# Kernel optimization log

Measured on AMD Instinct MI355X. Metric: run time of the kernel, lower is better.

## Reference

```python
import jax, jax.numpy as jnp
import numpy as np
from jax import lax

H = 1024; E = 512; V = 32000; WIN_D = 10.0; PAD = 0
S_LEN = 64; T_LEN = 64; B = 32


def _lstm_cell(x, h, c, W_ih, W_hh, b):
    z = x @ W_ih.T + h @ W_hh.T + b  # [B,4H], torch gate order i,f,g,o
    i, f, g, o = jnp.split(z, 4, axis=-1)
    c2 = jax.nn.sigmoid(f) * c + jax.nn.sigmoid(i) * jnp.tanh(g)
    h2 = jax.nn.sigmoid(o) * jnp.tanh(c2)
    return h2, c2


def setup_inputs() -> dict:
    key = jax.random.key(0)
    ks = jax.random.split(key, 24)
    sc = 0.05
    rn = lambda k, shape: (jax.random.normal(k, shape, jnp.float32) * sc)
    src_tokens = jax.random.randint(ks[0], (S_LEN, B), 0, V, dtype=jnp.int32)
    tgt_tokens = jax.random.randint(ks[1], (T_LEN, B), 1, V, dtype=jnp.int32)
    encode_len = jax.random.randint(ks[2], (B,), S_LEN // 2, S_LEN + 1, dtype=jnp.int32)
    encode_len = encode_len.at[0].set(S_LEN)  # pad_packed pads to max len
    return {
        "src_tokens": src_tokens, "tgt_tokens": tgt_tokens, "encode_len": encode_len,
        "emb_src": rn(ks[3], (V, E)), "emb_tar": rn(ks[4], (V, E)),
        "eW_ih0": rn(ks[5], (4 * H, E)), "eW_hh0": rn(ks[6], (4 * H, H)), "eb0": rn(ks[7], (4 * H,)),
        "eW_ih1": rn(ks[8], (4 * H, H)), "eW_hh1": rn(ks[9], (4 * H, H)), "eb1": rn(ks[10], (4 * H,)),
        "dW_ih0": rn(ks[11], (4 * H, E + H)), "dW_hh0": rn(ks[12], (4 * H, H)), "db0": rn(ks[13], (4 * H,)),
        "dW_ih1": rn(ks[14], (4 * H, H)), "dW_hh1": rn(ks[15], (4 * H, H)), "db1": rn(ks[16], (4 * H,)),
        "W_ht2tan": rn(ks[17], (H, H)), "w_tan2pt": rn(ks[18], (H,)),
        "W_ct2ht": rn(ks[19], (H, 2 * H)), "W_final": rn(ks[20], (V, H)),
    }


def reference(src_tokens, tgt_tokens, encode_len, emb_src, emb_tar,
              eW_ih0, eW_hh0, eb0, eW_ih1, eW_hh1, eb1,
              dW_ih0, dW_hh0, db0, dW_ih1, dW_hh1, db1,
              W_ht2tan, w_tan2pt, W_ct2ht, W_final):
    S, Bsz = src_tokens.shape
    elen_f = encode_len.astype(jnp.float32)

    # ---- encoder (2-layer LSTM with packed-sequence semantics: state frozen past len) ----
    x = emb_src[src_tokens]  # [S,B,E]
    h0 = jnp.zeros((2, Bsz, H), jnp.float32)
    c0 = jnp.zeros((2, Bsz, H), jnp.float32)

    def enc_step(carry, xt_t):
        h, c = carry
        xt, t = xt_t
        valid = (t < encode_len)[:, None]  # [B,1] bool
        h0n, c0n = _lstm_cell(xt, h[0], c[0], eW_ih0, eW_hh0, eb0)
        h1n, c1n = _lstm_cell(h0n, h[1], c[1], eW_ih1, eW_hh1, eb1)
        hs = jnp.stack([h0n, h1n]); cs = jnp.stack([c0n, c1n])
        h_new = jnp.where(valid[None], hs, h)
        c_new = jnp.where(valid[None], cs, c)
        out = jnp.where(valid, h_new[1], 0.0)  # pad_packed zeros at pads
        return (h_new, c_new), out

    (hn, cn), enc_out = lax.scan(enc_step, (h0, c0), (x, jnp.arange(S)))
    encode_h = enc_out.transpose(1, 0, 2)  # [B,S,H]
    positions = jnp.arange(S, dtype=jnp.float32)  # per_s / S matrix rows

    # ---- decoder loop (input-feeding: concat(y_t, ht)) with Gaussian-window local attention ----
    y = emb_tar[tgt_tokens]  # [T,B,E]

    def dec_step(carry, y_t):
        hd, cd, ht = carry
        inp = jnp.concatenate([y_t, ht], axis=-1)  # [B,E+H]
        h0n, c0n = _lstm_cell(inp, hd[0], cd[0], dW_ih0, dW_hh0, db0)
        h1n, c1n = _lstm_cell(h0n, hd[1], cd[1], dW_ih1, dW_hh1, db1)
        yt = h1n  # [B,H]
        pt = jax.nn.sigmoid(jnp.tanh(yt @ W_ht2tan.T) @ w_tan2pt) * elen_f  # [B]
        scores = jnp.einsum('bh,bsh->bs', yt, encode_h)
        scores = jnp.where(positions[None, :] < elen_f[:, None], scores, -jnp.inf)
        align = jax.nn.softmax(scores, axis=-1)
        window = jnp.exp(-((positions[None, :] - pt[:, None]) ** 2) / (WIN_D * WIN_D / 2.0))
        at = align * window  # [B,S]
        ct = jnp.einsum('bs,bsh->bh', at, encode_h)
        ht_new = jnp.tanh(jnp.concatenate([ct, yt], axis=-1) @ W_ct2ht.T)
        return (jnp.stack([h0n, h1n]), jnp.stack([c0n, c1n]), ht_new), ht_new

    init = (hn, cn, jnp.zeros((Bsz, H), jnp.float32))
    _, dec_out = lax.scan(dec_step, init, y)  # [T,B,H]

    P = jax.nn.log_softmax(dec_out @ W_final.T, axis=-1)  # [T,B,V]
    logp = jnp.take_along_axis(P[:-1], tgt_tokens[1:, :, None], axis=-1)[..., 0]
    tar_mask = (tgt_tokens[1:] != PAD).astype(jnp.float32)
    return (logp * tar_mask).sum(axis=0)  # [B]
```

## Files before the change

kernel.cpp:

```cpp
#include <hip/hip_runtime.h>
#include <math.h>

#define S_LEN 64
#define T_LEN 64
#define BSZ   32
#define EDIM  512
#define HDIM  1024
#define VDIM  32000
#define FOURH 4096

typedef __attribute__((ext_vector_type(8))) short  short8;
typedef __attribute__((ext_vector_type(4))) float  floatx4;

__device__ __forceinline__ unsigned short f2bf(float x){
  unsigned u = __float_as_uint(x);
  u = (u + 0x7FFFu + ((u >> 16) & 1u)) >> 16;
  return (unsigned short)u;
}
__device__ __forceinline__ float sigm(float x){ return 1.f/(1.f+__expf(-x)); }

__global__ void cvt_bf16_v4(const float* __restrict__ in, unsigned short* __restrict__ out, long n4){
  long i = (long)blockIdx.x*blockDim.x + threadIdx.x;
  long stride = (long)gridDim.x*blockDim.x;
  for (; i < n4; i += stride){
    float4 v = ((const float4*)in)[i];
    ushort4 o; o.x=f2bf(v.x); o.y=f2bf(v.y); o.z=f2bf(v.z); o.w=f2bf(v.w);
    ((ushort4*)out)[i] = o;
  }
}

__global__ void embed_gather(const int* __restrict__ toks, const float* __restrict__ emb,
                             unsigned short* __restrict__ out, int total4){
  int i = blockIdx.x*blockDim.x + threadIdx.x;
  if (i >= total4) return;
  const int e4 = EDIM/4;
  int r = i / e4, e = (i % e4)*4;
  int tok = toks[r];
  float4 v = *(const float4*)(emb + (size_t)tok*EDIM + e);
  ushort4 o; o.x=f2bf(v.x); o.y=f2bf(v.y); o.z=f2bf(v.z); o.w=f2bf(v.w);
  *(ushort4*)(out + (size_t)r*EDIM + e) = o;
}

__global__ void tok_row_kernel(const int* __restrict__ tgt, int* __restrict__ tokRow){
  int r = blockIdx.x*blockDim.x + threadIdx.x;
  if (r >= T_LEN*BSZ) return;
  int t = r >> 5, b = r & 31;
  tokRow[r] = (t < T_LEN-1) ? tgt[(t+1)*BSZ + b] : -1;
}

template<int EPI>
__global__ __launch_bounds__(256,1) void gemm_mfma(
    const unsigned short* __restrict__ A, int lda,
    const unsigned short* __restrict__ W, int ldw,
    const float* __restrict__ bias,
    float* __restrict__ C, int ldc, int K,
    float* __restrict__ rowSum, float* __restrict__ logitTgt, const int* __restrict__ tokRow)
{
  __shared__ unsigned short As[128*32];
  __shared__ unsigned short Ws[128*32];
  const int tid  = threadIdx.x;
  const int wave = tid >> 6, lane = tid & 63;
  const int bm = blockIdx.x * 128, bn = blockIdx.y * 128;
  const int wr = (wave >> 1) * 64, wc = (wave & 1) * 64;
  const int srow = tid >> 2, scol = (tid & 3) * 8;
  const int rg = (lane >> 4) * 8, rl = lane & 15;
  floatx4 acc[4][4] = {};

  for (int kt = 0; kt < K; kt += 32){
    short8 a0 = *(const short8*)(A + (size_t)(bm + srow)*lda      + kt + scol);
    short8 a1 = *(const short8*)(A + (size_t)(bm + 64 + srow)*lda + kt + scol);
    short8 w0 = *(const short8*)(W + (size_t)(bn + srow)*ldw      + kt + scol);
    short8 w1 = *(const short8*)(W + (size_t)(bn + 64 + srow)*ldw + kt + scol);
    __syncthreads();
    *(short8*)&As[srow*32 + scol]      = a0;
    *(short8*)&As[(64+srow)*32 + scol] = a1;
    *(short8*)&Ws[srow*32 + scol]      = w0;
    *(short8*)&Ws[(64+srow)*32 + scol] = w1;
    __syncthreads();
    short8 af[4], wf[4];
    #pragma unroll
    for (int m=0;m<4;m++) af[m] = *(const short8*)&As[(wr + m*16 + rl)*32 + rg];
    #pragma unroll
    for (int n=0;n<4;n++) wf[n] = *(const short8*)&Ws[(wc + n*16 + rl)*32 + rg];
    #pragma unroll
    for (int m=0;m<4;m++)
      #pragma unroll
      for (int n=0;n<4;n++)
        acc[m][n] = __builtin_amdgcn_mfma_f32_16x16x32_bf16(af[m], wf[n], acc[m][n], 0, 0, 0);
  }

  if (EPI == 0){
    float bv[4];
    #pragma unroll
    for (int n=0;n<4;n++) bv[n] = bias[bn + wc + n*16 + rl];
    #pragma unroll
    for (int m=0;m<4;m++){
      #pragma unroll
      for (int j=0;j<4;j++){
        int r = bm + wr + m*16 + (lane>>4)*4 + j;
        #pragma unroll
        for (int n=0;n<4;n++){
          int c = bn + wc + n*16 + rl;
          C[(size_t)r*ldc + c] = acc[m][n][j] + bv[n];
        }
      }
    }
  } else {
    #pragma unroll
    for (int m=0;m<4;m++){
      #pragma unroll
      for (int j=0;j<4;j++){
        int r = bm + wr + m*16 + (lane>>4)*4 + j;
        int tok = tokRow[r];
        float esum = 0.f;
        #pragma unroll
        for (int n=0;n<4;n++){
          int c = bn + wc + n*16 + rl;
          float v = acc[m][n][j];
          if (c == tok) logitTgt[r] = v;
          esum += __expf(v);
        }
        esum += __shfl_xor(esum, 1);
        esum += __shfl_xor(esum, 2);
        esum += __shfl_xor(esum, 4);
        esum += __shfl_xor(esum, 8);
        if (rl == 0) atomicAdd(&rowSum[r], esum);
      }
    }
  }
}

__global__ __launch_bounds__(256,1) void enc_l0_kernel(
    const float* __restrict__ preZ, const float* __restrict__ Whh,
    const float* __restrict__ h0, const float* __restrict__ c0,
    float* __restrict__ h0t, float* __restrict__ c0t, int t)
{
  const int wave = threadIdx.x >> 6, lane = threadIdx.x & 63;
  const int i = blockIdx.x*4 + wave;
  const int kb = lane*16;
  float4 wv[4][4];
  #pragma unroll
  for (int g=0; g<4; g++){
    const float* wrow = Whh + (size_t)(g*HDIM + i)*HDIM + kb;
    #pragma unroll
    for (int q=0;q<4;q++) wv[g][q] = *(const float4*)(wrow + q*4);
  }
  for (int b=0; b<BSZ; b++){
    const float* hp = h0 + b*HDIM + kb;
    float4 hv[4];
    #pragma unroll
    for (int q=0;q<4;q++) hv[q] = *(const float4*)(hp + q*4);
    float s0=0,s1=0,s2=0,s3=0;
    #pragma unroll
    for (int q=0;q<4;q++){
      s0 += wv[0][q].x*hv[q].x + wv[0][q].y*hv[q].y + wv[0][q].z*hv[q].z + wv[0][q].w*hv[q].w;
      s1 += wv[1][q].x*hv[q].x + wv[1][q].y*hv[q].y + wv[1][q].z*hv[q].z + wv[1][q].w*hv[q].w;
      s2 += wv[2][q].x*hv[q].x + wv[2][q].y*hv[q].y + wv[2][q].z*hv[q].z + wv[2][q].w*hv[q].w;
      s3 += wv[3][q].x*hv[q].x + wv[3][q].y*hv[q].y + wv[3][q].z*hv[q].z + wv[3][q].w*hv[q].w;
    }
    #pragma unroll
    for (int off=1; off<64; off<<=1){
      s0 += __shfl_xor(s0, off); s1 += __shfl_xor(s1, off);
      s2 += __shfl_xor(s2, off); s3 += __shfl_xor(s3, off);
    }
    if (lane == 0){
      const float* pz = preZ + (size_t)(t*BSZ + b)*FOURH;
      float zi = pz[i] + s0, zf = pz[HDIM+i] + s1, zg = pz[2*HDIM+i] + s2, zo = pz[3*HDIM+i] + s3;
      float cc = sigm(zf)*c0[b*HDIM+i] + sigm(zi)*tanhf(zg);
      float hh = sigm(zo)*tanhf(cc);
      h0t[b*HDIM+i] = hh; c0t[b*HDIM+i] = cc;
    }
  }
}

__global__ __launch_bounds__(256,1) void enc_l1_kernel(
    const float* __restrict__ Wih, const float* __restrict__ Whh, const float* __restrict__ bias,
    const float* __restrict__ h0t, const float* __restrict__ c0t,
    const float* __restrict__ h1, const float* __restrict__ c1,
    const float* __restrict__ h0p, const float* __restrict__ c0p,
    float* __restrict__ h0n, float* __restrict__ c0n,
    float* __restrict__ h1n, float* __restrict__ c1n,
    float* __restrict__ ench, const int* __restrict__ elen, int t)
{
  const int wave = threadIdx.x >> 6, lane = threadIdx.x & 63;
  const int i = blockIdx.x*4 + wave;
  const int kb = lane*16;
  float4 wi[4][4], wh[4][4];
  #pragma unroll
  for (int g=0; g<4; g++){
    const float* r1 = Wih + (size_t)(g*HDIM + i)*HDIM + kb;
    const float* r2 = Whh + (size_t)(g*HDIM + i)*HDIM + kb;
    #pragma unroll
    for (int q=0;q<4;q++){ wi[g][q] = *(const float4*)(r1 + q*4); wh[g][q] = *(const float4*)(r2 + q*4); }
  }
  float bz0 = bias[i], bz1 = bias[HDIM+i], bz2 = bias[2*HDIM+i], bz3 = bias[3*HDIM+i];
  for (int b=0; b<BSZ; b++){
    const float* xp = h0t + b*HDIM + kb;
    const float* hp = h1  + b*HDIM + kb;
    float4 xv[4], hv[4];
    #pragma unroll
    for (int q=0;q<4;q++){ xv[q] = *(const float4*)(xp + q*4); hv[q] = *(const float4*)(hp + q*4); }
    float s0=0,s1=0,s2=0,s3=0;
    #pragma unroll
    for (int q=0;q<4;q++){
      s0 += wi[0][q].x*xv[q].x + wi[0][q].y*xv[q].y + wi[0][q].z*xv[q].z + wi[0][q].w*xv[q].w
          + wh[0][q].x*hv[q].x + wh[0][q].y*hv[q].y + wh[0][q].z*hv[q].z + wh[0][q].w*hv[q].w;
      s1 += wi[1][q].x*xv[q].x + wi[1][q].y*xv[q].y + wi[1][q].z*xv[q].z + wi[1][q].w*xv[q].w
          + wh[1][q].x*hv[q].x + wh[1][q].y*hv[q].y + wh[1][q].z*hv[q].z + wh[1][q].w*hv[q].w;
      s2 += wi[2][q].x*xv[q].x + wi[2][q].y*xv[q].y + wi[2][q].z*xv[q].z + wi[2][q].w*xv[q].w
          + wh[2][q].x*hv[q].x + wh[2][q].y*hv[q].y + wh[2][q].z*hv[q].z + wh[2][q].w*hv[q].w;
      s3 += wi[3][q].x*xv[q].x + wi[3][q].y*xv[q].y + wi[3][q].z*xv[q].z + wi[3][q].w*xv[q].w
          + wh[3][q].x*hv[q].x + wh[3][q].y*hv[q].y + wh[3][q].z*hv[q].z + wh[3][q].w*hv[q].w;
    }
    #pragma unroll
    for (int off=1; off<64; off<<=1){
      s0 += __shfl_xor(s0, off); s1 += __shfl_xor(s1, off);
      s2 += __shfl_xor(s2, off); s3 += __shfl_xor(s3, off);
    }
    if (lane == 0){
      float zi = bz0+s0, zf = bz1+s1, zg = bz2+s2, zo = bz3+s3;
      float cc = sigm(zf)*c1[b*HDIM+i] + sigm(zi)*tanhf(zg);
      float hh = sigm(zo)*tanhf(cc);
      bool valid = t < elen[b];
      size_t bi = (size_t)b*HDIM + i;
      if (valid){
        h0n[bi] = h0t[bi]; c0n[bi] = c0t[bi]; h1n[bi] = hh; c1n[bi] = cc;
        ench[((size_t)t*BSZ + b)*HDIM + i] = hh;
      } else {
        h0n[bi] = h0p[bi]; c0n[bi] = c0p[bi]; h1n[bi] = h1[bi]; c1n[bi] = c1[bi];
        ench[((size_t)t*BSZ + b)*HDIM + i] = 0.f;
      }
    }
  }
}

__global__ __launch_bounds__(256,1) void dec_l0_kernel(
    const float* __restrict__ preZ, const float* __restrict__ Wih, const float* __restrict__ Whh,
    const float* __restrict__ ht, const float* __restrict__ hd0, const float* __restrict__ cd0,
    float* __restrict__ h0t, float* __restrict__ c0t, int t)
{
  const int wave = threadIdx.x >> 6, lane = threadIdx.x & 63;
  const int i = blockIdx.x*4 + wave;
  const int kb = lane*16;
  float4 wi[4][4], wh[4][4];
  #pragma unroll
  for (int g=0; g<4; g++){
    const float* r1 = Wih + (size_t)(g*HDIM + i)*(EDIM+HDIM) + EDIM + kb;
    const float* r2 = Whh + (size_t)(g*HDIM + i)*HDIM + kb;
    #pragma unroll
    for (int q=0;q<4;q++){ wi[g][q] = *(const float4*)(r1 + q*4); wh[g][q] = *(const float4*)(r2 + q*4); }
  }
  for (int b=0; b<BSZ; b++){
    const float* xp = ht  + b*HDIM + kb;
    const float* hp = hd0 + b*HDIM + kb;
    float4 xv[4], hv[4];
    #pragma unroll
    for (int q=0;q<4;q++){ xv[q] = *(const float4*)(xp + q*4); hv[q] = *(const float4*)(hp + q*4); }
    float s0=0,s1=0,s2=0,s3=0;
    #pragma unroll
    for (int q=0;q<4;q++){
      s0 += wi[0][q].x*xv[q].x + wi[0][q].y*xv[q].y + wi[0][q].z*xv[q].z + wi[0][q].w*xv[q].w
          + wh[0][q].x*hv[q].x + wh[0][q].y*hv[q].y + wh[0][q].z*hv[q].z + wh[0][q].w*hv[q].w;
      s1 += wi[1][q].x*xv[q].x + wi[1][q].y*xv[q].y + wi[1][q].z*xv[q].z + wi[1][q].w*xv[q].w
          + wh[1][q].x*hv[q].x + wh[1][q].y*hv[q].y + wh[1][q].z*hv[q].z + wh[1][q].w*hv[q].w;
      s2 += wi[2][q].x*xv[q].x + wi[2][q].y*xv[q].y + wi[2][q].z*xv[q].z + wi[2][q].w*xv[q].w
          + wh[2][q].x*hv[q].x + wh[2][q].y*hv[q].y + wh[2][q].z*hv[q].z + wh[2][q].w*hv[q].w;
      s3 += wi[3][q].x*xv[q].x + wi[3][q].y*xv[q].y + wi[3][q].z*xv[q].z + wi[3][q].w*xv[q].w
          + wh[3][q].x*hv[q].x + wh[3][q].y*hv[q].y + wh[3][q].z*hv[q].z + wh[3][q].w*hv[q].w;
    }
    #pragma unroll
    for (int off=1; off<64; off<<=1){
      s0 += __shfl_xor(s0, off); s1 += __shfl_xor(s1, off);
      s2 += __shfl_xor(s2, off); s3 += __shfl_xor(s3, off);
    }
    if (lane == 0){
      const float* pz = preZ + (size_t)(t*BSZ + b)*FOURH;
      float zi = pz[i]+s0, zf = pz[HDIM+i]+s1, zg = pz[2*HDIM+i]+s2, zo = pz[3*HDIM+i]+s3;
      float cc = sigm(zf)*cd0[b*HDIM+i] + sigm(zi)*tanhf(zg);
      float hh = sigm(zo)*tanhf(cc);
      h0t[b*HDIM+i] = hh; c0t[b*HDIM+i] = cc;
    }
  }
}

__global__ __launch_bounds__(256,1) void dec_l1_kernel(
    const float* __restrict__ Wih, const float* __restrict__ Whh, const float* __restrict__ bias,
    const float* __restrict__ h0t, const float* __restrict__ c0t,
    const float* __restrict__ h1, const float* __restrict__ c1,
    float* __restrict__ h0n, float* __restrict__ c0n,
    float* __restrict__ h1n, float* __restrict__ c1n,
    float* __restrict__ yt)
{
  const int wave = threadIdx.x >> 6, lane = threadIdx.x & 63;
  const int i = blockIdx.x*4 + wave;
  const int kb = lane*16;
  float4 wi[4][4], wh[4][4];
  #pragma unroll
  for (int g=0; g<4; g++){
    const float* r1 = Wih + (size_t)(g*HDIM + i)*HDIM + kb;
    const float* r2 = Whh + (size_t)(g*HDIM + i)*HDIM + kb;
    #pragma unroll
    for (int q=0;q<4;q++){ wi[g][q] = *(const float4*)(r1 + q*4); wh[g][q] = *(const float4*)(r2 + q*4); }
  }
  float bz0 = bias[i], bz1 = bias[HDIM+i], bz2 = bias[2*HDIM+i], bz3 = bias[3*HDIM+i];
  for (int b=0; b<BSZ; b++){
    const float* xp = h0t + b*HDIM + kb;
    const float* hp = h1  + b*HDIM + kb;
    float4 xv[4], hv[4];
    #pragma unroll
    for (int q=0;q<4;q++){ xv[q] = *(const float4*)(xp + q*4); hv[q] = *(const float4*)(hp + q*4); }
    float s0=0,s1=0,s2=0,s3=0;
    #pragma unroll
    for (int q=0;q<4;q++){
      s0 += wi[0][q].x*xv[q].x + wi[0][q].y*xv[q].y + wi[0][q].z*xv[q].z + wi[0][q].w*xv[q].w
          + wh[0][q].x*hv[q].x + wh[0][q].y*hv[q].y + wh[0][q].z*hv[q].z + wh[0][q].w*hv[q].w;
      s1 += wi[1][q].x*xv[q].x + wi[1][q].y*xv[q].y + wi[1][q].z*xv[q].z + wi[1][q].w*xv[q].w
          + wh[1][q].x*hv[q].x + wh[1][q].y*hv[q].y + wh[1][q].z*hv[q].z + wh[1][q].w*hv[q].w;
      s2 += wi[2][q].x*xv[q].x + wi[2][q].y*xv[q].y + wi[2][q].z*xv[q].z + wi[2][q].w*xv[q].w
          + wh[2][q].x*hv[q].x + wh[2][q].y*hv[q].y + wh[2][q].z*hv[q].z + wh[2][q].w*hv[q].w;
      s3 += wi[3][q].x*xv[q].x + wi[3][q].y*xv[q].y + wi[3][q].z*xv[q].z + wi[3][q].w*xv[q].w
          + wh[3][q].x*hv[q].x + wh[3][q].y*hv[q].y + wh[3][q].z*hv[q].z + wh[3][q].w*hv[q].w;
    }
    #pragma unroll
    for (int off=1; off<64; off<<=1){
      s0 += __shfl_xor(s0, off); s1 += __shfl_xor(s1, off);
      s2 += __shfl_xor(s2, off); s3 += __shfl_xor(s3, off);
    }
    if (lane == 0){
      float zi = bz0+s0, zf = bz1+s1, zg = bz2+s2, zo = bz3+s3;
      float cc = sigm(zf)*c1[b*HDIM+i] + sigm(zi)*tanhf(zg);
      float hh = sigm(zo)*tanhf(cc);
      size_t bi = (size_t)b*HDIM + i;
      h0n[bi] = h0t[bi]; c0n[bi] = c0t[bi]; h1n[bi] = hh; c1n[bi] = cc;
      yt[bi] = hh;
    }
  }
}

__global__ __launch_bounds__(256,1) void dec_attn_a(
    const float* __restrict__ Wht, const float* __restrict__ yt, const float* __restrict__ ench,
    float* __restrict__ tanv, float* __restrict__ scores)
{
  const int wave = threadIdx.x >> 6, lane = threadIdx.x & 63;
  const int wid = blockIdx.x*4 + wave;
  const int kb = lane*16;
  if (wid < HDIM){
    const int i = wid;
    float4 wv[4];
    #pragma unroll
    for (int q=0;q<4;q++) wv[q] = *(const float4*)(Wht + (size_t)i*HDIM + kb + q*4);
    for (int b=0; b<BSZ; b++){
      const float* hp = yt + b*HDIM + kb;
      float s = 0;
      #pragma unroll
      for (int q=0;q<4;q++){
        float4 hv = *(const float4*)(hp + q*4);
        s += wv[q].x*hv.x + wv[q].y*hv.y + wv[q].z*hv.z + wv[q].w*hv.w;
      }
      #pragma unroll
      for (int off=1; off<64; off<<=1) s += __shfl_xor(s, off);
      if (lane == 0) tanv[b*HDIM + i] = tanhf(s);
    }
  } else {
    const int sid = wid - HDIM;
    const int b = sid >> 6, s_idx = sid & 63;
    const float* yp = yt + b*HDIM + kb;
    const float* ep = ench + ((size_t)s_idx*BSZ + b)*HDIM + kb;
    float s = 0;
    #pragma unroll
    for (int q=0;q<4;q++){
      float4 yv = *(const float4*)(yp + q*4);
      float4 ev = *(const float4*)(ep + q*4);
      s += yv.x*ev.x + yv.y*ev.y + yv.z*ev.z + yv.w*ev.w;
    }
    #pragma unroll
    for (int off=1; off<64; off<<=1) s += __shfl_xor(s, off);
    if (lane == 0) scores[b*S_LEN + s_idx] = s;
  }
}

__global__ __launch_bounds__(256,1) void dec_attn_b(
    const float* __restrict__ tanv, const float* __restrict__ w_tan2pt,
    const float* __restrict__ scores, const int* __restrict__ elen,
    const float* __restrict__ ench, float* __restrict__ ct)
{
  const int b = blockIdx.x, tid = threadIdx.x;
  __shared__ float red[256];
  __shared__ float atS[S_LEN];
  __shared__ float ptS;
  float part = 0;
  for (int k = tid; k < HDIM; k += 256) part += tanv[b*HDIM + k]*w_tan2pt[k];
  red[tid] = part; __syncthreads();
  for (int off = 128; off; off >>= 1){ if (tid < off) red[tid] += red[tid+off]; __syncthreads(); }
  if (tid == 0) ptS = sigm(red[0]) * (float)elen[b];
  __syncthreads();
  if (tid < 64){
    int L = elen[b];
    float sc = (tid < L) ? scores[b*S_LEN + tid] : -1e30f;
    float m = sc;
    #pragma unroll
    for (int off=1; off<64; off<<=1) m = fmaxf(m, __shfl_xor(m, off));
    float e = (tid < L) ? __expf(sc - m) : 0.f;
    float ssum = e;
    #pragma unroll
    for (int off=1; off<64; off<<=1) ssum += __shfl_xor(ssum, off);
    float d = (float)tid - ptS;
    atS[tid] = (e/ssum) * __expf(-(d*d)*(1.0f/50.0f));
  }
  __syncthreads();
  const int h0 = tid*4;
  float4 acc = {0,0,0,0};
  for (int s = 0; s < S_LEN; s++){
    float a = atS[s];
    float4 v = *(const float4*)(ench + ((size_t)s*BSZ + b)*HDIM + h0);
    acc.x += a*v.x; acc.y += a*v.y; acc.z += a*v.z; acc.w += a*v.w;
  }
  *(float4*)(ct + b*HDIM + h0) = acc;
}

__global__ __launch_bounds__(256,1) void dec_attn_c(
    const float* __restrict__ Wct, const float* __restrict__ ct, const float* __restrict__ yt,
    float* __restrict__ htn, unsigned short* __restrict__ decoutb, int t)
{
  const int wave = threadIdx.x >> 6, lane = threadIdx.x & 63;
  const int i = blockIdx.x*4 + wave;
  float4 wv[8];
  #pragma unroll
  for (int q=0;q<8;q++) wv[q] = *(const float4*)(Wct + (size_t)i*(2*HDIM) + lane*32 + q*4);
  const float* xsrc = (lane < 32) ? ct : yt;
  const int col = (lane & 31) * 32;
  for (int b=0; b<BSZ; b++){
    const float* xp = xsrc + b*HDIM + col;
    float s = 0;
    #pragma unroll
    for (int q=0;q<8;q++){
      float4 xv = *(const float4*)(xp + q*4);
      s += wv[q].x*xv.x + wv[q].y*xv.y + wv[q].z*xv.z + wv[q].w*xv.w;
    }
    #pragma unroll
    for (int off=1; off<64; off<<=1) s += __shfl_xor(s, off);
    if (lane == 0){
      float v = tanhf(s);
      htn[(size_t)b*HDIM + i] = v;
      decoutb[((size_t)t*BSZ + b)*HDIM + i] = f2bf(v);
    }
  }
}

__global__ void loss_kernel(const float* __restrict__ rowSum, const float* __restrict__ logitTgt,
                            const int* __restrict__ tgt, float* __restrict__ out)
{
  const int b = blockIdx.x, t = threadIdx.x;
  float v = 0.f;
  if (t < T_LEN-1){
    int r = t*BSZ + b;
    if (tgt[(t+1)*BSZ + b] != 0) v = logitTgt[r] - logf(rowSum[r]);
  }
  #pragma unroll
  for (int off=1; off<64; off<<=1) v += __shfl_xor(v, off);
  if (t == 0) out[b] = v;
}

extern "C" void kernel_launch(void* const* d_in, const int* in_sizes, int n_in,
                              void* d_out, int out_size, void* d_ws, size_t ws_size,
                              hipStream_t stream)
{
  const int*   src_tokens = (const int*)d_in[0];
  const int*   tgt_tokens = (const int*)d_in[1];
  const int*   encode_len = (const int*)d_in[2];
  const float* emb_src  = (const float*)d_in[3];
  const float* emb_tar  = (const float*)d_in[4];
  const float* eW_ih0   = (const float*)d_in[5];
  const float* eW_hh0   = (const float*)d_in[6];
  const float* eb0      = (const float*)d_in[7];
  const float* eW_ih1   = (const float*)d_in[8];
  const float* eW_hh1   = (const float*)d_in[9];
  const float* eb1      = (const float*)d_in[10];
  const float* dW_ih0   = (const float*)d_in[11];
  const float* dW_hh0   = (const float*)d_in[12];
  const float* db0      = (const float*)d_in[13];
  const float* dW_ih1   = (const float*)d_in[14];
  const float* dW_hh1   = (const float*)d_in[15];
  const float* db1      = (const float*)d_in[16];
  const float* W_ht2tan = (const float*)d_in[17];
  const float* w_tan2pt = (const float*)d_in[18];
  const float* W_ct2ht  = (const float*)d_in[19];
  const float* W_final  = (const float*)d_in[20];
  float* out = (float*)d_out;

  char* wsp = (char*)d_ws;
  auto alloc = [&](size_t bytes)->void*{
    void* p = (void*)wsp; wsp += ((bytes + 255) & ~(size_t)255); return p;
  };
  float* preZe = (float*)alloc(2048ull*4096*4);
  float* preZd = (float*)alloc(2048ull*4096*4);
  float* ench  = (float*)alloc((size_t)S_LEN*BSZ*HDIM*4);
  float* h0s   = (float*)alloc(2ull*BSZ*HDIM*4);
  float* c0s   = (float*)alloc(2ull*BSZ*HDIM*4);
  float* h1s   = (float*)alloc(2ull*BSZ*HDIM*4);
  float* c1s   = (float*)alloc(2ull*BSZ*HDIM*4);
  float* hts   = (float*)alloc(2ull*BSZ*HDIM*4);
  float* h0t   = (float*)alloc((size_t)BSZ*HDIM*4);
  float* c0t   = (float*)alloc((size_t)BSZ*HDIM*4);
  float* ytb   = (float*)alloc((size_t)BSZ*HDIM*4);
  float* tanv  = (float*)alloc((size_t)BSZ*HDIM*4);
  float* ctb   = (float*)alloc((size_t)BSZ*HDIM*4);
  float* scores= (float*)alloc((size_t)BSZ*S_LEN*4);
  float* rowSum   = (float*)alloc(2048*4);
  float* logitTgt = (float*)alloc(2048*4);
  int*   tokRow   = (int*)alloc(2048*4);
  unsigned short* xsrc    = (unsigned short*)alloc(2048ull*EDIM*2);
  unsigned short* ytgt    = (unsigned short*)alloc(2048ull*EDIM*2);
  unsigned short* eWih0b  = (unsigned short*)alloc((size_t)FOURH*EDIM*2);
  unsigned short* dWih0b  = (unsigned short*)alloc((size_t)FOURH*(EDIM+HDIM)*2);
  unsigned short* Wfinb   = (unsigned short*)alloc((size_t)VDIM*HDIM*2);
  unsigned short* decoutb = (unsigned short*)alloc(2048ull*HDIM*2);

  const size_t ST = (size_t)BSZ*HDIM;

  hipMemsetAsync(h0s, 0, ST*4, stream);
  hipMemsetAsync(c0s, 0, ST*4, stream);
  hipMemsetAsync(h1s, 0, ST*4, stream);
  hipMemsetAsync(c1s, 0, ST*4, stream);
  hipMemsetAsync(hts, 0, ST*4, stream);
  hipMemsetAsync(rowSum, 0, 2048*4, stream);

  cvt_bf16_v4<<<1024, 256, 0, stream>>>(eW_ih0, eWih0b, (long)FOURH*EDIM/4);
  cvt_bf16_v4<<<2048, 256, 0, stream>>>(dW_ih0, dWih0b, (long)FOURH*(EDIM+HDIM)/4);
  cvt_bf16_v4<<<4096, 256, 0, stream>>>(W_final, Wfinb, (long)VDIM*HDIM/4);
  embed_gather<<<(2048*EDIM/4 + 255)/256, 256, 0, stream>>>(src_tokens, emb_src, xsrc, 2048*EDIM/4);
  embed_gather<<<(2048*EDIM/4 + 255)/256, 256, 0, stream>>>(tgt_tokens, emb_tar, ytgt, 2048*EDIM/4);
  tok_row_kernel<<<8, 256, 0, stream>>>(tgt_tokens, tokRow);

  gemm_mfma<0><<<dim3(16,32), 256, 0, stream>>>(xsrc, EDIM, eWih0b, EDIM, eb0,
                                                preZe, FOURH, EDIM, nullptr, nullptr, nullptr);
  gemm_mfma<0><<<dim3(16,32), 256, 0, stream>>>(ytgt, EDIM, dWih0b, EDIM+HDIM, db0,
                                                preZd, FOURH, EDIM, nullptr, nullptr, nullptr);

  for (int t = 0; t < S_LEN; t++){
    int p = t & 1;
    float *h0p = h0s + p*ST, *c0p = c0s + p*ST, *h1p = h1s + p*ST, *c1p = c1s + p*ST;
    float *h0n = h0s + (1-p)*ST, *c0n = c0s + (1-p)*ST, *h1n = h1s + (1-p)*ST, *c1n = c1s + (1-p)*ST;
    enc_l0_kernel<<<256, 256, 0, stream>>>(preZe, eW_hh0, h0p, c0p, h0t, c0t, t);
    enc_l1_kernel<<<256, 256, 0, stream>>>(eW_ih1, eW_hh1, eb1, h0t, c0t, h1p, c1p, h0p, c0p,
                                           h0n, c0n, h1n, c1n, ench, encode_len, t);
  }

  for (int t = 0; t < T_LEN; t++){
    int p = t & 1;
    float *h0p = h0s + p*ST, *c0p = c0s + p*ST, *h1p = h1s + p*ST, *c1p = c1s + p*ST;
    float *h0n = h0s + (1-p)*ST, *c0n = c0s + (1-p)*ST, *h1n = h1s + (1-p)*ST, *c1n = c1s + (1-p)*ST;
    float *htp = hts + p*ST, *htn = hts + (1-p)*ST;
    dec_l0_kernel<<<256, 256, 0, stream>>>(preZd, dW_ih0, dW_hh0, htp, h0p, c0p, h0t, c0t, t);
    dec_l1_kernel<<<256, 256, 0, stream>>>(dW_ih1, dW_hh1, db1, h0t, c0t, h1p, c1p,
                                           h0n, c0n, h1n, c1n, ytb);
    dec_attn_a<<<768, 256, 0, stream>>>(W_ht2tan, ytb, ench, tanv, scores);
    dec_attn_b<<<32, 256, 0, stream>>>(tanv, w_tan2pt, scores, encode_len, ench, ctb);
    dec_attn_c<<<256, 256, 0, stream>>>(W_ct2ht, ctb, ytb, htn, decoutb, t);
  }

  gemm_mfma<1><<<dim3(16,250), 256, 0, stream>>>(decoutb, HDIM, Wfinb, HDIM, nullptr,
                                                 nullptr, 0, HDIM, rowSum, logitTgt, tokRow);
  loss_kernel<<<32, 64, 0, stream>>>(rowSum, logitTgt, tgt_tokens, out);
}
```

Measured before the change: 18.20 ms.

## Fuse encoder/decoder recurrence into persistent megakernel with grid barriers

Replaces the per-timestep launches of LSTM layer and attention kernels (2 per encoder step, 5 per decoder step) with one persistent kernel of 256 blocks. Phases are separated by a software grid barrier built on atomics. Each wave now handles one hidden unit for 16 batch rows, and state buffers are updated in place instead of double-buffered. This removes kernel launch and drain overhead, but it relies on all 256 blocks being co-resident, and the barrier has a spin timeout that could silently break ordering.

```diff
diff --git a/kernel.cpp b/kernel.cpp
--- a/kernel.cpp
+++ b/kernel.cpp
@@ -9,6 +9,9 @@
 #define VDIM  32000
 #define FOURH 4096
 
+#define NBLK  256
+#define TPB   512
+
 typedef __attribute__((ext_vector_type(8))) short  short8;
 typedef __attribute__((ext_vector_type(4))) float  floatx4;
 
@@ -18,6 +21,38 @@
   return (unsigned short)u;
 }
 __device__ __forceinline__ float sigm(float x){ return 1.f/(1.f+__expf(-x)); }
+
+__device__ __forceinline__ float allred(float s){
+  #pragma unroll
+  for (int off=1; off<64; off<<=1) s += __shfl_xor(s, off);
+  return s;
+}
+__device__ __forceinline__ float allmax(float s){
+  #pragma unroll
+  for (int off=1; off<64; off<<=1) s = fmaxf(s, __shfl_xor(s, off));
+  return s;
+}
+
+__device__ __forceinline__ void gbar(unsigned* cnt, unsigned* gen){
+  __syncthreads();
+  if (threadIdx.x == 0){
+    __threadfence();
+    unsigned g = __hip_atomic_load(gen, __ATOMIC_RELAXED, __HIP_MEMORY_SCOPE_AGENT);
+    unsigned a = __hip_atomic_fetch_add(cnt, 1u, __ATOMIC_ACQ_REL, __HIP_MEMORY_SCOPE_AGENT);
+    if (a == (unsigned)(NBLK-1)){
+      __hip_atomic_store(cnt, 0u, __ATOMIC_RELAXED, __HIP_MEMORY_SCOPE_AGENT);
+      __hip_atomic_fetch_add(gen, 1u, __ATOMIC_RELEASE, __HIP_MEMORY_SCOPE_AGENT);
+    } else {
+      long it = 0;
+      while (__hip_atomic_load(gen, __ATOMIC_RELAXED, __HIP_MEMORY_SCOPE_AGENT) == g){
+        __builtin_amdgcn_s_sleep(1);
+        if (++it > (1L<<20)) break;
+      }
+    }
+    __threadfence();
+  }
+  __syncthreads();
+}
 
 __global__ void cvt_bf16_v4(const float* __restrict__ in, unsigned short* __restrict__ out, long n4){
   long i = (long)blockIdx.x*blockDim.x + threadIdx.x;
@@ -130,320 +165,300 @@
   }
 }
 
-__global__ __launch_bounds__(256,1) void enc_l0_kernel(
-    const float* __restrict__ preZ, const float* __restrict__ Whh,
-    const float* __restrict__ h0, const float* __restrict__ c0,
-    float* __restrict__ h0t, float* __restrict__ c0t, int t)
+__global__ __launch_bounds__(TPB, 2) void megakernel(
+    const float* __restrict__ preZe, const float* __restrict__ preZd,
+    const float* __restrict__ eW_hh0,
+    const float* __restrict__ eW_ih1, const float* __restrict__ eW_hh1, const float* __restrict__ eb1,
+    const float* __restrict__ dW_ih0, const float* __restrict__ dW_hh0,
+    const float* __restrict__ dW_ih1, const float* __restrict__ dW_hh1, const float* __restrict__ db1,
+    const float* __restrict__ Wht, const float* __restrict__ w2pt, const float* __restrict__ Wct,
+    const int* __restrict__ elen,
+    float* __restrict__ h0, float* __restrict__ c0,
+    float* __restrict__ h1, float* __restrict__ c1,
+    float* __restrict__ h0t, float* __restrict__ c0t,
+    float* __restrict__ ht,  float* __restrict__ ench,
+    float* __restrict__ tanv, float* __restrict__ scores, float* __restrict__ ct,
+    unsigned short* __restrict__ decoutb,
+    unsigned* cnt, unsigned* gen)
 {
-  const int wave = threadIdx.x >> 6, lane = threadIdx.x & 63;
-  const int i = blockIdx.x*4 + wave;
-  const int kb = lane*16;
-  float4 wv[4][4];
-  #pragma unroll
-  for (int g=0; g<4; g++){
-    const float* wrow = Whh + (size_t)(g*HDIM + i)*HDIM + kb;
-    #pragma unroll
-    for (int q=0;q<4;q++) wv[g][q] = *(const float4*)(wrow + q*4);
-  }
-  for (int b=0; b<BSZ; b++){
-    const float* hp = h0 + b*HDIM + kb;
-    float4 hv[4];
-    #pragma unroll
-    for (int q=0;q<4;q++) hv[q] = *(const float4*)(hp + q*4);
-    float s0=0,s1=0,s2=0,s3=0;
-    #pragma unroll
-    for (int q=0;q<4;q++){
-      s0 += wv[0][q].x*hv[q].x + wv[0][q].y*hv[q].y + wv[0][q].z*hv[q].z + wv[0][q].w*hv[q].w;
-      s1 += wv[1][q].x*hv[q].x + wv[1][q].y*hv[q].y + wv[1][q].z*hv[q].z + wv[1][q].w*hv[q].w;
-      s2 += wv[2][q].x*hv[q].x + wv[2][q].y*hv[q].y + wv[2][q].z*hv[q].z + wv[2][q].w*hv[q].w;
-      s3 += wv[3][q].x*hv[q].x + wv[3][q].y*hv[q].y + wv[3][q].z*hv[q].z + wv[3][q].w*hv[q].w;
-    }
-    #pragma unroll
-    for (int off=1; off<64; off<<=1){
-      s0 += __shfl_xor(s0, off); s1 += __shfl_xor(s1, off);
-      s2 += __shfl_xor(s2, off); s3 += __shfl_xor(s3, off);
-    }
-    if (lane == 0){
-      const float* pz = preZ + (size_t)(t*BSZ + b)*FOURH;
-      float zi = pz[i] + s0, zf = pz[HDIM+i] + s1, zg = pz[2*HDIM+i] + s2, zo = pz[3*HDIM+i] + s3;
-      float cc = sigm(zf)*c0[b*HDIM+i] + sigm(zi)*tanhf(zg);
-      float hh = sigm(zo)*tanhf(cc);
-      h0t[b*HDIM+i] = hh; c0t[b*HDIM+i] = cc;
-    }
-  }
-}
-
-__global__ __launch_bounds__(256,1) void enc_l1_kernel(
-    const float* __restrict__ Wih, const float* __restrict__ Whh, const float* __restrict__ bias,
-    const float* __restrict__ h0t, const float* __restrict__ c0t,
-    const float* __restrict__ h1, const float* __restrict__ c1,
-    const float* __restrict__ h0p, const float* __restrict__ c0p,
-    float* __restrict__ h0n, float* __restrict__ c0n,
-    float* __restrict__ h1n, float* __restrict__ c1n,
-    float* __restrict__ ench, const int* __restrict__ elen, int t)
-{
-  const int wave = threadIdx.x >> 6, lane = threadIdx.x & 63;
-  const int i = blockIdx.x*4 + wave;
-  const int kb = lane*16;
-  float4 wi[4][4], wh[4][4];
-  #pragma unroll
-  for (int g=0; g<4; g++){
-    const float* r1 = Wih + (size_t)(g*HDIM + i)*HDIM + kb;
-    const float* r2 = Whh + (size_t)(g*HDIM + i)*HDIM + kb;
-    #pragma unroll
-    for (int q=0;q<4;q++){ wi[g][q] = *(const float4*)(r1 + q*4); wh[g][q] = *(const float4*)(r2 + q*4); }
-  }
-  float bz0 = bias[i], bz1 = bias[HDIM+i], bz2 = bias[2*HDIM+i], bz3 = bias[3*HDIM+i];
-  for (int b=0; b<BSZ; b++){
-    const float* xp = h0t + b*HDIM + kb;
-    const float* hp = h1  + b*HDIM + kb;
-    float4 xv[4], hv[4];
-    #pragma unroll
-    for (int q=0;q<4;q++){ xv[q] = *(const float4*)(xp + q*4); hv[q] = *(const float4*)(hp + q*4); }
-    float s0=0,s1=0,s2=0,s3=0;
-    #pragma unroll
-    for (int q=0;q<4;q++){
-      s0 += wi[0][q].x*xv[q].x + wi[0][q].y*xv[q].y + wi[0][q].z*xv[q].z + wi[0][q].w*xv[q].w
-          + wh[0][q].x*hv[q].x + wh[0][q].y*hv[q].y + wh[0][q].z*hv[q].z + wh[0][q].w*hv[q].w;
-      s1 += wi[1][q].x*xv[q].x + wi[1][q].y*xv[q].y + wi[1][q].z*xv[q].z + wi[1][q].w*xv[q].w
-          + wh[1][q].x*hv[q].x + wh[1][q].y*hv[q].y + wh[1][q].z*hv[q].z + wh[1][q].w*hv[q].w;
-      s2 += wi[2][q].x*xv[q].x + wi[2][q].y*xv[q].y + wi[2][q].z*xv[q].z + wi[2][q].w*xv[q].w
-          + wh[2][q].x*hv[q].x + wh[2][q].y*hv[q].y + wh[2][q].z*hv[q].z + wh[2][q].w*hv[q].w;
-      s3 += wi[3][q].x*xv[q].x + wi[3][q].y*xv[q].y + wi[3][q].z*xv[q].z + wi[3][q].w*xv[q].w
-          + wh[3][q].x*hv[q].x + wh[3][q].y*hv[q].y + wh[3][q].z*hv[q].z + wh[3][q].w*hv[q].w;
-    }
-    #pragma unroll
-    for (int off=1; off<64; off<<=1){
-      s0 += __shfl_xor(s0, off); s1 += __shfl_xor(s1, off);
-      s2 += __shfl_xor(s2, off); s3 += __shfl_xor(s3, off);
-    }
-    if (lane == 0){
-      float zi = bz0+s0, zf = bz1+s1, zg = bz2+s2, zo = bz3+s3;
-      float cc = sigm(zf)*c1[b*HDIM+i] + sigm(zi)*tanhf(zg);
-      float hh = sigm(zo)*tanhf(cc);
-      bool valid = t < elen[b];
-      size_t bi = (size_t)b*HDIM + i;
-      if (valid){
-        h0n[bi] = h0t[bi]; c0n[bi] = c0t[bi]; h1n[bi] = hh; c1n[bi] = cc;
-        ench[((size_t)t*BSZ + b)*HDIM + i] = hh;
-      } else {
-        h0n[bi] = h0p[bi]; c0n[bi] = c0p[bi]; h1n[bi] = h1[bi]; c1n[bi] = c1[bi];
-        ench[((size_t)t*BSZ + b)*HDIM + i] = 0.f;
-      }
-    }
-  }
-}
-
-__global__ __launch_bounds__(256,1) void dec_l0_kernel(
-    const float* __restrict__ preZ, const float* __restrict__ Wih, const float* __restrict__ Whh,
-    const float* __restrict__ ht, const float* __restrict__ hd0, const float* __restrict__ cd0,
-    float* __restrict__ h0t, float* __restrict__ c0t, int t)
-{
-  const int wave = threadIdx.x >> 6, lane = threadIdx.x & 63;
-  const int i = blockIdx.x*4 + wave;
-  const int kb = lane*16;
-  float4 wi[4][4], wh[4][4];
-  #pragma unroll
-  for (int g=0; g<4; g++){
-    const float* r1 = Wih + (size_t)(g*HDIM + i)*(EDIM+HDIM) + EDIM + kb;
-    const float* r2 = Whh + (size_t)(g*HDIM + i)*HDIM + kb;
-    #pragma unroll
-    for (int q=0;q<4;q++){ wi[g][q] = *(const float4*)(r1 + q*4); wh[g][q] = *(const float4*)(r2 + q*4); }
-  }
-  for (int b=0; b<BSZ; b++){
-    const float* xp = ht  + b*HDIM + kb;
-    const float* hp = hd0 + b*HDIM + kb;
-    float4 xv[4], hv[4];
-    #pragma unroll
-    for (int q=0;q<4;q++){ xv[q] = *(const float4*)(xp + q*4); hv[q] = *(const float4*)(hp + q*4); }
-    float s0=0,s1=0,s2=0,s3=0;
-    #pragma unroll
-    for (int q=0;q<4;q++){
-      s0 += wi[0][q].x*xv[q].x + wi[0][q].y*xv[q].y + wi[0][q].z*xv[q].z + wi[0][q].w*xv[q].w
-          + wh[0][q].x*hv[q].x + wh[0][q].y*hv[q].y + wh[0][q].z*hv[q].z + wh[0][q].w*hv[q].w;
-      s1 += wi[1][q].x*xv[q].x + wi[1][q].y*xv[q].y + wi[1][q].z*xv[q].z + wi[1][q].w*xv[q].w
-          + wh[1][q].x*hv[q].x + wh[1][q].y*hv[q].y + wh[1][q].z*hv[q].z + wh[1][q].w*hv[q].w;
-      s2 += wi[2][q].x*xv[q].x + wi[2][q].y*xv[q].y + wi[2][q].z*xv[q].z + wi[2][q].w*xv[q].w
-          + wh[2][q].x*hv[q].x + wh[2][q].y*hv[q].y + wh[2][q].z*hv[q].z + wh[2][q].w*hv[q].w;
-      s3 += wi[3][q].x*xv[q].x + wi[3][q].y*xv[q].y + wi[3][q].z*xv[q].z + wi[3][q].w*xv[q].w
-          + wh[3][q].x*hv[q].x + wh[3][q].y*hv[q].y + wh[3][q].z*hv[q].z + wh[3][q].w*hv[q].w;
-    }
-    #pragma unroll
-    for (int off=1; off<64; off<<=1){
-      s0 += __shfl_xor(s0, off); s1 += __shfl_xor(s1, off);
-      s2 += __shfl_xor(s2, off); s3 += __shfl_xor(s3, off);
-    }
-    if (lane == 0){
-      const float* pz = preZ + (size_t)(t*BSZ + b)*FOURH;
-      float zi = pz[i]+s0, zf = pz[HDIM+i]+s1, zg = pz[2*HDIM+i]+s2, zo = pz[3*HDIM+i]+s3;
-      float cc = sigm(zf)*cd0[b*HDIM+i] + sigm(zi)*tanhf(zg);
-      float hh = sigm(zo)*tanhf(cc);
-      h0t[b*HDIM+i] = hh; c0t[b*HDIM+i] = cc;
-    }
-  }
-}
-
-__global__ __launch_bounds__(256,1) void dec_l1_kernel(
-    const float* __restrict__ Wih, const float* __restrict__ Whh, const float* __restrict__ bias,
-    const float* __restrict__ h0t, const float* __restrict__ c0t,
-    const float* __restrict__ h1, const float* __restrict__ c1,
-    float* __restrict__ h0n, float* __restrict__ c0n,
-    float* __restrict__ h1n, float* __restrict__ c1n,
-    float* __restrict__ yt)
-{
-  const int wave = threadIdx.x >> 6, lane = threadIdx.x & 63;
-  const int i = blockIdx.x*4 + wave;
-  const int kb = lane*16;
-  float4 wi[4][4], wh[4][4];
-  #pragma unroll
-  for (int g=0; g<4; g++){
-    const float* r1 = Wih + (size_t)(g*HDIM + i)*HDIM + kb;
-    const float* r2 = Whh + (size_t)(g*HDIM + i)*HDIM + kb;
-    #pragma unroll
-    for (int q=0;q<4;q++){ wi[g][q] = *(const float4*)(r1 + q*4); wh[g][q] = *(const float4*)(r2 + q*4); }
-  }
-  float bz0 = bias[i], bz1 = bias[HDIM+i], bz2 = bias[2*HDIM+i], bz3 = bias[3*HDIM+i];
-  for (int b=0; b<BSZ; b++){
-    const float* xp = h0t + b*HDIM + kb;
-    const float* hp = h1  + b*HDIM + kb;
-    float4 xv[4], hv[4];
-    #pragma unroll
-    for (int q=0;q<4;q++){ xv[q] = *(const float4*)(xp + q*4); hv[q] = *(const float4*)(hp + q*4); }
-    float s0=0,s1=0,s2=0,s3=0;
-    #pragma unroll
-    for (int q=0;q<4;q++){
-      s0 += wi[0][q].x*xv[q].x + wi[0][q].y*xv[q].y + wi[0][q].z*xv[q].z + wi[0][q].w*xv[q].w
-          + wh[0][q].x*hv[q].x + wh[0][q].y*hv[q].y + wh[0][q].z*hv[q].z + wh[0][q].w*hv[q].w;
-      s1 += wi[1][q].x*xv[q].x + wi[1][q].y*xv[q].y + wi[1][q].z*xv[q].z + wi[1][q].w*xv[q].w
-          + wh[1][q].x*hv[q].x + wh[1][q].y*hv[q].y + wh[1][q].z*hv[q].z + wh[1][q].w*hv[q].w;
-      s2 += wi[2][q].x*xv[q].x + wi[2][q].y*xv[q].y + wi[2][q].z*xv[q].z + wi[2][q].w*xv[q].w
-          + wh[2][q].x*hv[q].x + wh[2][q].y*hv[q].y + wh[2][q].z*hv[q].z + wh[2][q].w*hv[q].w;
-      s3 += wi[3][q].x*xv[q].x + wi[3][q].y*xv[q].y + wi[3][q].z*xv[q].z + wi[3][q].w*xv[q].w
-          + wh[3][q].x*hv[q].x + wh[3][q].y*hv[q].y + wh[3][q].z*hv[q].z + wh[3][q].w*hv[q].w;
-    }
-    #pragma unroll
-    for (int off=1; off<64; off<<=1){
-      s0 += __shfl_xor(s0, off); s1 += __shfl_xor(s1, off);
-      s2 += __shfl_xor(s2, off); s3 += __shfl_xor(s3, off);
-    }
-    if (lane == 0){
-      float zi = bz0+s0, zf = bz1+s1, zg = bz2+s2, zo = bz3+s3;
-      float cc = sigm(zf)*c1[b*HDIM+i] + sigm(zi)*tanhf(zg);
-      float hh = sigm(zo)*tanhf(cc);
-      size_t bi = (size_t)b*HDIM + i;
-      h0n[bi] = h0t[bi]; c0n[bi] = c0t[bi]; h1n[bi] = hh; c1n[bi] = cc;
-      yt[bi] = hh;
-    }
-  }
-}
-
-__global__ __launch_bounds__(256,1) void dec_attn_a(
-    const float* __restrict__ Wht, const float* __restrict__ yt, const float* __restrict__ ench,
-    float* __restrict__ tanv, float* __restrict__ scores)
-{
-  const int wave = threadIdx.x >> 6, lane = threadIdx.x & 63;
-  const int wid = blockIdx.x*4 + wave;
-  const int kb = lane*16;
-  if (wid < HDIM){
-    const int i = wid;
-    float4 wv[4];
-    #pragma unroll
-    for (int q=0;q<4;q++) wv[q] = *(const float4*)(Wht + (size_t)i*HDIM + kb + q*4);
-    for (int b=0; b<BSZ; b++){
-      const float* hp = yt + b*HDIM + kb;
-      float s = 0;
+  const int tid  = threadIdx.x;
+  const int lane = tid & 63;
+  const int gw   = blockIdx.x*(TPB/64) + (tid >> 6);
+  const int j    = gw >> 1;
+  const int bb   = (gw & 1) * 16;
+
+  for (int t = 0; t < S_LEN; t++){
+    {
+      float4 w[4][4];
+      #pragma unroll
+      for (int g=0; g<4; g++){
+        const float* r = eW_hh0 + ((size_t)(g*HDIM + j))*HDIM + lane*16;
+        #pragma unroll
+        for (int q=0;q<4;q++) w[g][q] = *(const float4*)(r + q*4);
+      }
+      for (int ib=0; ib<16; ib++){
+        const int b = bb + ib;
+        float pz0=0,pz1=0,pz2=0,pz3=0,cv=0;
+        if (lane == 0){
+          const float* pz = preZe + ((size_t)(t*BSZ + b))*FOURH + j;
+          pz0 = pz[0]; pz1 = pz[HDIM]; pz2 = pz[2*HDIM]; pz3 = pz[3*HDIM];
+          cv = c0[b*HDIM + j];
+        }
+        const float* hp = h0 + b*HDIM + lane*16;
+        float4 hv[4];
+        #pragma unroll
+        for (int q=0;q<4;q++) hv[q] = *(const float4*)(hp + q*4);
+        float s0=0,s1=0,s2=0,s3=0;
+        #pragma unroll
+        for (int q=0;q<4;q++){
+          s0 += w[0][q].x*hv[q].x + w[0][q].y*hv[q].y + w[0][q].z*hv[q].z + w[0][q].w*hv[q].w;
+          s1 += w[1][q].x*hv[q].x + w[1][q].y*hv[q].y + w[1][q].z*hv[q].z + w[1][q].w*hv[q].w;
+          s2 += w[2][q].x*hv[q].x + w[2][q].y*hv[q].y + w[2][q].z*hv[q].z + w[2][q].w*hv[q].w;
+          s3 += w[3][q].x*hv[q].x + w[3][q].y*hv[q].y + w[3][q].z*hv[q].z + w[3][q].w*hv[q].w;
+        }
+        s0 = allred(s0); s1 = allred(s1); s2 = allred(s2); s3 = allred(s3);
+        if (lane == 0){
+          float cc = sigm(pz1+s1)*cv + sigm(pz0+s0)*tanhf(pz2+s2);
+          float hh = sigm(pz3+s3)*tanhf(cc);
+          h0t[b*HDIM+j] = hh; c0t[b*HDIM+j] = cc;
+        }
+      }
+    }
+    gbar(cnt, gen);
+    {
+      float4 wi[4][4], wh[4][4];
+      #pragma unroll
+      for (int g=0; g<4; g++){
+        const float* r1 = eW_ih1 + ((size_t)(g*HDIM + j))*HDIM + lane*16;
+        const float* r2 = eW_hh1 + ((size_t)(g*HDIM + j))*HDIM + lane*16;
+        #pragma unroll
+        for (int q=0;q<4;q++){ wi[g][q] = *(const float4*)(r1 + q*4); wh[g][q] = *(const float4*)(r2 + q*4); }
+      }
+      float b0=0,b1=0,b2=0,b3=0;
+      if (lane == 0){ b0=eb1[j]; b1=eb1[HDIM+j]; b2=eb1[2*HDIM+j]; b3=eb1[3*HDIM+j]; }
+      for (int ib=0; ib<16; ib++){
+        const int b = bb + ib;
+        float c1v=0, h0tv=0, c0tv=0; int lenb=0;
+        if (lane == 0){
+          size_t bi = (size_t)b*HDIM + j;
+          c1v = c1[bi]; h0tv = h0t[bi]; c0tv = c0t[bi]; lenb = elen[b];
+        }
+        const float* xp = h0t + b*HDIM + lane*16;
+        const float* hp = h1  + b*HDIM + lane*16;
+        float4 xv[4], hv[4];
+        #pragma unroll
+        for (int q=0;q<4;q++){ xv[q] = *(const float4*)(xp + q*4); hv[q] = *(const float4*)(hp + q*4); }
+        float s0=0,s1=0,s2=0,s3=0;
+        #pragma unroll
+        for (int q=0;q<4;q++){
+          s0 += wi[0][q].x*xv[q].x + wi[0][q].y*xv[q].y + wi[0][q].z*xv[q].z + wi[0][q].w*xv[q].w
+              + wh[0][q].x*hv[q].x + wh[0][q].y*hv[q].y + wh[0][q].z*hv[q].z + wh[0][q].w*hv[q].w;
+          s1 += wi[1][q].x*xv[q].x + wi[1][q].y*xv[q].y + wi[1][q].z*xv[q].z + wi[1][q].w*xv[q].w
+              + wh[1][q].x*hv[q].x + wh[1][q].y*hv[q].y + wh[1][q].z*hv[q].z + wh[1][q].w*hv[q].w;
+          s2 += wi[2][q].x*xv[q].x + wi[2][q].y*xv[q].y + wi[2][q].z*xv[q].z + wi[2][q].w*xv[q].w
+              + wh[2][q].x*hv[q].x + wh[2][q].y*hv[q].y + wh[2][q].z*hv[q].z + wh[2][q].w*hv[q].w;
+          s3 += wi[3][q].x*xv[q].x + wi[3][q].y*xv[q].y + wi[3][q].z*xv[q].z + wi[3][q].w*xv[q].w
+              + wh[3][q].x*hv[q].x + wh[3][q].y*hv[q].y + wh[3][q].z*hv[q].z + wh[3][q].w*hv[q].w;
+        }
+        s0 = allred(s0); s1 = allred(s1); s2 = allred(s2); s3 = allred(s3);
+        if (lane == 0){
+          float cc = sigm(b1+s1)*c1v + sigm(b0+s0)*tanhf(b2+s2);
+          float hh = sigm(b3+s3)*tanhf(cc);
+          size_t bi = (size_t)b*HDIM + j;
+          float eout = 0.f;
+          if (t < lenb){
+            h1[bi] = hh; c1[bi] = cc; h0[bi] = h0tv; c0[bi] = c0tv;
+            eout = hh;
+          }
+          ench[((size_t)t*BSZ + b)*HDIM + j] = eout;
+        }
+      }
+    }
+    gbar(cnt, gen);
+  }
+
+  for (int t = 0; t < T_LEN; t++){
+    {
+      float4 wi[4][4], wh[4][4];
+      #pragma unroll
+      for (int g=0; g<4; g++){
+        const float* r1 = dW_ih0 + ((size_t)(g*HDIM + j))*(EDIM+HDIM) + EDIM + lane*16;
+        const float* r2 = dW_hh0 + ((size_t)(g*HDIM + j))*HDIM + lane*16;
+        #pragma unroll
+        for (int q=0;q<4;q++){ wi[g][q] = *(const float4*)(r1 + q*4); wh[g][q] = *(const float4*)(r2 + q*4); }
+      }
+      for (int ib=0; ib<16; ib++){
+        const int b = bb + ib;
+        float pz0=0,pz1=0,pz2=0,pz3=0,cv=0;
+        if (lane == 0){
+          const float* pz = preZd + ((size_t)(t*BSZ + b))*FOURH + j;
+          pz0 = pz[0]; pz1 = pz[HDIM]; pz2 = pz[2*HDIM]; pz3 = pz[3*HDIM];
+          cv = c0[b*HDIM + j];
+        }
+        const float* xp = ht + b*HDIM + lane*16;
+        const float* hp = h0 + b*HDIM + lane*16;
+        float4 xv[4], hv[4];
+        #pragma unroll
+        for (int q=0;q<4;q++){ xv[q] = *(const float4*)(xp + q*4); hv[q] = *(const float4*)(hp + q*4); }
+        float s0=0,s1=0,s2=0,s3=0;
+        #pragma unroll
+        for (int q=0;q<4;q++){
+          s0 += wi[0][q].x*xv[q].x + wi[0][q].y*xv[q].y + wi[0][q].z*xv[q].z + wi[0][q].w*xv[q].w
+              + wh[0][q].x*hv[q].x + wh[0][q].y*hv[q].y + wh[0][q].z*hv[q].z + wh[0][q].w*hv[q].w;
+          s1 += wi[1][q].x*xv[q].x + wi[1][q].y*xv[q].y + wi[1][q].z*xv[q].z + wi[1][q].w*xv[q].w
+              + wh[1][q].x*hv[q].x + wh[1][q].y*hv[q].y + wh[1][q].z*hv[q].z + wh[1][q].w*hv[q].w;
+          s2 += wi[2][q].x*xv[q].x + wi[2][q].y*xv[q].y + wi[2][q].z*xv[q].z + wi[2][q].w*xv[q].w
+              + wh[2][q].x*hv[q].x + wh[2][q].y*hv[q].y + wh[2][q].z*hv[q].z + wh[2][q].w*hv[q].w;
+          s3 += wi[3][q].x*xv[q].x + wi[3][q].y*xv[q].y + wi[3][q].z*xv[q].z + wi[3][q].w*xv[q].w
+              + wh[3][q].x*hv[q].x + wh[3][q].y*hv[q].y + wh[3][q].z*hv[q].z + wh[3][q].w*hv[q].w;
+        }
+        s0 = allred(s0); s1 = allred(s1); s2 = allred(s2); s3 = allred(s3);
+        if (lane == 0){
+          float cc = sigm(pz1+s1)*cv + sigm(pz0+s0)*tanhf(pz2+s2);
+          float hh = sigm(pz3+s3)*tanhf(cc);
+          h0t[b*HDIM+j] = hh; c0t[b*HDIM+j] = cc;
+        }
+      }
+    }
+    gbar(cnt, gen);
+    {
+      float4 wi[4][4], wh[4][4];
+      #pragma unroll
+      for (int g=0; g<4; g++){
+        const float* r1 = dW_ih1 + ((size_t)(g*HDIM + j))*HDIM + lane*16;
+        const float* r2 = dW_hh1 + ((size_t)(g*HDIM + j))*HDIM + lane*16;
+        #pragma unroll
+        for (int q=0;q<4;q++){ wi[g][q] = *(const float4*)(r1 + q*4); wh[g][q] = *(const float4*)(r2 + q*4); }
+      }
+      float b0=0,b1=0,b2=0,b3=0;
+      if (lane == 0){ b0=db1[j]; b1=db1[HDIM+j]; b2=db1[2*HDIM+j]; b3=db1[3*HDIM+j]; }
+      for (int ib=0; ib<16; ib++){
+        const int b = bb + ib;
+        float c1v=0, h0tv=0, c0tv=0;
+        if (lane == 0){
+          size_t bi = (size_t)b*HDIM + j;
+          c1v = c1[bi]; h0tv = h0t[bi]; c0tv = c0t[bi];
+        }
+        const float* xp = h0t + b*HDIM + lane*16;
+        const float* hp = h1  + b*HDIM + lane*16;
+        float4 xv[4], hv[4];
+        #pragma unroll
+        for (int q=0;q<4;q++){ xv[q] = *(const float4*)(xp + q*4); hv[q] = *(const float4*)(hp + q*4); }
+        float s0=0,s1=0,s2=0,s3=0;
+        #pragma unroll
+        for (int q=0;q<4;q++){
+          s0 += wi[0][q].x*xv[q].x + wi[0][q].y*xv[q].y + wi[0][q].z*xv[q].z + wi[0][q].w*xv[q].w
+              + wh[0][q].x*hv[q].x + wh[0][q].y*hv[q].y + wh[0][q].z*hv[q].z + wh[0][q].w*hv[q].w;
+          s1 += wi[1][q].x*xv[q].x + wi[1][q].y*xv[q].y + wi[1][q].z*xv[q].z + wi[1][q].w*xv[q].w
+              + wh[1][q].x*hv[q].x + wh[1][q].y*hv[q].y + wh[1][q].z*hv[q].z + wh[1][q].w*hv[q].w;
+          s2 += wi[2][q].x*xv[q].x + wi[2][q].y*xv[q].y + wi[2][q].z*xv[q].z + wi[2][q].w*xv[q].w
+              + wh[2][q].x*hv[q].x + wh[2][q].y*hv[q].y + wh[2][q].z*hv[q].z + wh[2][q].w*hv[q].w;
+          s3 += wi[3][q].x*xv[q].x + wi[3][q].y*xv[q].y + wi[3][q].z*xv[q].z + wi[3][q].w*xv[q].w
+              + wh[3][q].x*hv[q].x + wh[3][q].y*hv[q].y + wh[3][q].z*hv[q].z + wh[3][q].w*hv[q].w;
+        }
+        s0 = allred(s0); s1 = allred(s1); s2 = allred(s2); s3 = allred(s3);
+        if (lane == 0){
+          float cc = sigm(b1+s1)*c1v + sigm(b0+s0)*tanhf(b2+s2);
+          float hh = sigm(b3+s3)*tanhf(cc);
+          size_t bi = (size_t)b*HDIM + j;
+          h1[bi] = hh; c1[bi] = cc; h0[bi] = h0tv; c0[bi] = c0tv;
+        }
+      }
+    }
+    gbar(cnt, gen);
+    {
+      {
+        const int b2 = gw >> 6, s2 = gw & 63;
+        int lenb = 0;
+        if (lane == 0) lenb = elen[b2];
+        const float* yp = h1 + b2*HDIM + lane*16;
+        const float* ep = ench + ((size_t)s2*BSZ + b2)*HDIM + lane*16;
+        float s = 0;
+        #pragma unroll
+        for (int q=0;q<4;q++){
+          float4 yv = *(const float4*)(yp + q*4);
+          float4 ev = *(const float4*)(ep + q*4);
+          s += yv.x*ev.x + yv.y*ev.y + yv.z*ev.z + yv.w*ev.w;
+        }
+        s = allred(s);
+        if (lane == 0) scores[b2*S_LEN + s2] = (s2 < lenb) ? s : -1e30f;
+      }
+      {
+        float4 w[4];
+        #pragma unroll
+        for (int q=0;q<4;q++) w[q] = *(const float4*)(Wht + (size_t)j*HDIM + lane*16 + q*4);
+        for (int ib=0; ib<16; ib++){
+          const int b = bb + ib;
+          const float* hp = h1 + b*HDIM + lane*16;
+          float s = 0;
+          #pragma unroll
+          for (int q=0;q<4;q++){
+            float4 hv = *(const float4*)(hp + q*4);
+            s += w[q].x*hv.x + w[q].y*hv.y + w[q].z*hv.z + w[q].w*hv.w;
+          }
+          s = allred(s);
+          if (lane == 0) tanv[b*HDIM + j] = tanhf(s);
+        }
+      }
+    }
+    gbar(cnt, gen);
+    if (gw < 512){
+      const int b = gw >> 4;
+      const int hb = (gw & 15) * 64;
+      float part = 0;
+      const float* tv = tanv + b*HDIM + lane*16;
+      const float* wp = w2pt + lane*16;
       #pragma unroll
       for (int q=0;q<4;q++){
-        float4 hv = *(const float4*)(hp + q*4);
-        s += wv[q].x*hv.x + wv[q].y*hv.y + wv[q].z*hv.z + wv[q].w*hv.w;
-      }
-      #pragma unroll
-      for (int off=1; off<64; off<<=1) s += __shfl_xor(s, off);
-      if (lane == 0) tanv[b*HDIM + i] = tanhf(s);
-    }
-  } else {
-    const int sid = wid - HDIM;
-    const int b = sid >> 6, s_idx = sid & 63;
-    const float* yp = yt + b*HDIM + kb;
-    const float* ep = ench + ((size_t)s_idx*BSZ + b)*HDIM + kb;
-    float s = 0;
-    #pragma unroll
-    for (int q=0;q<4;q++){
-      float4 yv = *(const float4*)(yp + q*4);
-      float4 ev = *(const float4*)(ep + q*4);
-      s += yv.x*ev.x + yv.y*ev.y + yv.z*ev.z + yv.w*ev.w;
-    }
-    #pragma unroll
-    for (int off=1; off<64; off<<=1) s += __shfl_xor(s, off);
-    if (lane == 0) scores[b*S_LEN + s_idx] = s;
-  }
-}
-
-__global__ __launch_bounds__(256,1) void dec_attn_b(
-    const float* __restrict__ tanv, const float* __restrict__ w_tan2pt,
-    const float* __restrict__ scores, const int* __restrict__ elen,
-    const float* __restrict__ ench, float* __restrict__ ct)
-{
-  const int b = blockIdx.x, tid = threadIdx.x;
-  __shared__ float red[256];
-  __shared__ float atS[S_LEN];
-  __shared__ float ptS;
-  float part = 0;
-  for (int k = tid; k < HDIM; k += 256) part += tanv[b*HDIM + k]*w_tan2pt[k];
-  red[tid] = part; __syncthreads();
-  for (int off = 128; off; off >>= 1){ if (tid < off) red[tid] += red[tid+off]; __syncthreads(); }
-  if (tid == 0) ptS = sigm(red[0]) * (float)elen[b];
-  __syncthreads();
-  if (tid < 64){
-    int L = elen[b];
-    float sc = (tid < L) ? scores[b*S_LEN + tid] : -1e30f;
-    float m = sc;
-    #pragma unroll
-    for (int off=1; off<64; off<<=1) m = fmaxf(m, __shfl_xor(m, off));
-    float e = (tid < L) ? __expf(sc - m) : 0.f;
-    float ssum = e;
-    #pragma unroll
-    for (int off=1; off<64; off<<=1) ssum += __shfl_xor(ssum, off);
-    float d = (float)tid - ptS;
-    atS[tid] = (e/ssum) * __expf(-(d*d)*(1.0f/50.0f));
-  }
-  __syncthreads();
-  const int h0 = tid*4;
-  float4 acc = {0,0,0,0};
-  for (int s = 0; s < S_LEN; s++){
-    float a = atS[s];
-    float4 v = *(const float4*)(ench + ((size_t)s*BSZ + b)*HDIM + h0);
-    acc.x += a*v.x; acc.y += a*v.y; acc.z += a*v.z; acc.w += a*v.w;
-  }
-  *(float4*)(ct + b*HDIM + h0) = acc;
-}
-
-__global__ __launch_bounds__(256,1) void dec_attn_c(
-    const float* __restrict__ Wct, const float* __restrict__ ct, const float* __restrict__ yt,
-    float* __restrict__ htn, unsigned short* __restrict__ decoutb, int t)
-{
-  const int wave = threadIdx.x >> 6, lane = threadIdx.x & 63;
-  const int i = blockIdx.x*4 + wave;
-  float4 wv[8];
-  #pragma unroll
-  for (int q=0;q<8;q++) wv[q] = *(const float4*)(Wct + (size_t)i*(2*HDIM) + lane*32 + q*4);
-  const float* xsrc = (lane < 32) ? ct : yt;
-  const int col = (lane & 31) * 32;
-  for (int b=0; b<BSZ; b++){
-    const float* xp = xsrc + b*HDIM + col;
-    float s = 0;
-    #pragma unroll
-    for (int q=0;q<8;q++){
-      float4 xv = *(const float4*)(xp + q*4);
-      s += wv[q].x*xv.x + wv[q].y*xv.y + wv[q].z*xv.z + wv[q].w*xv.w;
-    }
-    #pragma unroll
-    for (int off=1; off<64; off<<=1) s += __shfl_xor(s, off);
-    if (lane == 0){
-      float v = tanhf(s);
-      htn[(size_t)b*HDIM + i] = v;
-      decoutb[((size_t)t*BSZ + b)*HDIM + i] = f2bf(v);
-    }
+        float4 a = *(const float4*)(tv + q*4);
+        float4 c = *(const float4*)(wp + q*4);
+        part += a.x*c.x + a.y*c.y + a.z*c.z + a.w*c.w;
+      }
+      part = allred(part);
+      float ptv = sigm(part) * (float)elen[b];
+      float sc = scores[b*S_LEN + lane];
+      float m = allmax(sc);
+      float e = __expf(sc - m);
+      float ssum = allred(e);
+      float d = (float)lane - ptv;
+      float atl = (e/ssum) * __expf(-(d*d)*0.02f);
+      float acc = 0;
+      #pragma unroll 4
+      for (int s = 0; s < S_LEN; s++){
+        float a = __shfl(atl, s);
+        acc += a * ench[((size_t)s*BSZ + b)*HDIM + hb + lane];
+      }
+      ct[b*HDIM + hb + lane] = acc;
+    }
+    gbar(cnt, gen);
+    {
+      float4 wc_[4], wy_[4];
+      #pragma unroll
+      for (int q=0;q<4;q++){
+        wc_[q] = *(const float4*)(Wct + (size_t)j*(2*HDIM) + lane*16 + q*4);
+        wy_[q] = *(const float4*)(Wct + (size_t)j*(2*HDIM) + HDIM + lane*16 + q*4);
+      }
+      for (int ib=0; ib<16; ib++){
+        const int b = bb + ib;
+        const float* cp = ct + b*HDIM + lane*16;
+        const float* yp = h1 + b*HDIM + lane*16;
+        float s = 0;
+        #pragma unroll
+        for (int q=0;q<4;q++){
+          float4 cv = *(const float4*)(cp + q*4);
+          float4 yv = *(const float4*)(yp + q*4);
+          s += wc_[q].x*cv.x + wc_[q].y*cv.y + wc_[q].z*cv.z + wc_[q].w*cv.w
+             + wy_[q].x*yv.x + wy_[q].y*yv.y + wy_[q].z*yv.z + wy_[q].w*yv.w;
+        }
+        s = allred(s);
+        if (lane == 0){
+          float v = tanhf(s);
+          ht[(size_t)b*HDIM + j] = v;
+          decoutb[((size_t)t*BSZ + b)*HDIM + j] = f2bf(v);
+        }
+      }
+    }
+    gbar(cnt, gen);
   }
 }
 
@@ -495,20 +510,20 @@
   float* preZe = (float*)alloc(2048ull*4096*4);
   float* preZd = (float*)alloc(2048ull*4096*4);
   float* ench  = (float*)alloc((size_t)S_LEN*BSZ*HDIM*4);
-  float* h0s   = (float*)alloc(2ull*BSZ*HDIM*4);
-  float* c0s   = (float*)alloc(2ull*BSZ*HDIM*4);
-  float* h1s   = (float*)alloc(2ull*BSZ*HDIM*4);
-  float* c1s   = (float*)alloc(2ull*BSZ*HDIM*4);
-  float* hts   = (float*)alloc(2ull*BSZ*HDIM*4);
+  float* h0    = (float*)alloc((size_t)BSZ*HDIM*4);
+  float* c0    = (float*)alloc((size_t)BSZ*HDIM*4);
+  float* h1    = (float*)alloc((size_t)BSZ*HDIM*4);
+  float* c1    = (float*)alloc((size_t)BSZ*HDIM*4);
+  float* ht    = (float*)alloc((size_t)BSZ*HDIM*4);
   float* h0t   = (float*)alloc((size_t)BSZ*HDIM*4);
   float* c0t   = (float*)alloc((size_t)BSZ*HDIM*4);
-  float* ytb   = (float*)alloc((size_t)BSZ*HDIM*4);
   float* tanv  = (float*)alloc((size_t)BSZ*HDIM*4);
   float* ctb   = (float*)alloc((size_t)BSZ*HDIM*4);
   float* scores= (float*)alloc((size_t)BSZ*S_LEN*4);
   float* rowSum   = (float*)alloc(2048*4);
   float* logitTgt = (float*)alloc(2048*4);
   int*   tokRow   = (int*)alloc(2048*4);
+  unsigned* barws = (unsigned*)alloc(256);
   unsigned short* xsrc    = (unsigned short*)alloc(2048ull*EDIM*2);
   unsigned short* ytgt    = (unsigned short*)alloc(2048ull*EDIM*2);
   unsigned short* eWih0b  = (unsigned short*)alloc((size_t)FOURH*EDIM*2);
@@ -518,12 +533,13 @@
 
   const size_t ST = (size_t)BSZ*HDIM;
 
-  hipMemsetAsync(h0s, 0, ST*4, stream);
-  hipMemsetAsync(c0s, 0, ST*4, stream);
-  hipMemsetAsync(h1s, 0, ST*4, stream);
-  hipMemsetAsync(c1s, 0, ST*4, stream);
-  hipMemsetAsync(hts, 0, ST*4, stream);
+  hipMemsetAsync(h0, 0, ST*4, stream);
+  hipMemsetAsync(c0, 0, ST*4, stream);
+  hipMemsetAsync(h1, 0, ST*4, stream);
+  hipMemsetAsync(c1, 0, ST*4, stream);
+  hipMemsetAsync(ht, 0, ST*4, stream);
   hipMemsetAsync(rowSum, 0, 2048*4, stream);
+  hipMemsetAsync(barws, 0, 256, stream);
 
   cvt_bf16_v4<<<1024, 256, 0, stream>>>(eW_ih0, eWih0b, (long)FOURH*EDIM/4);
   cvt_bf16_v4<<<2048, 256, 0, stream>>>(dW_ih0, dWih0b, (long)FOURH*(EDIM+HDIM)/4);
@@ -537,27 +553,12 @@
   gemm_mfma<0><<<dim3(16,32), 256, 0, stream>>>(ytgt, EDIM, dWih0b, EDIM+HDIM, db0,
                                                 preZd, FOURH, EDIM, nullptr, nullptr, nullptr);
 
-  for (int t = 0; t < S_LEN; t++){
-    int p = t & 1;
-    float *h0p = h0s + p*ST, *c0p = c0s + p*ST, *h1p = h1s + p*ST, *c1p = c1s + p*ST;
-    float *h0n = h0s + (1-p)*ST, *c0n = c0s + (1-p)*ST, *h1n = h1s + (1-p)*ST, *c1n = c1s + (1-p)*ST;
-    enc_l0_kernel<<<256, 256, 0, stream>>>(preZe, eW_hh0, h0p, c0p, h0t, c0t, t);
-    enc_l1_kernel<<<256, 256, 0, stream>>>(eW_ih1, eW_hh1, eb1, h0t, c0t, h1p, c1p, h0p, c0p,
-                                           h0n, c0n, h1n, c1n, ench, encode_len, t);
-  }
-
-  for (int t = 0; t < T_LEN; t++){
-    int p = t & 1;
-    float *h0p = h0s + p*ST, *c0p = c0s + p*ST, *h1p = h1s + p*ST, *c1p = c1s + p*ST;
-    float *h0n = h0s + (1-p)*ST, *c0n = c0s + (1-p)*ST, *h1n = h1s + (1-p)*ST, *c1n = c1s + (1-p)*ST;
-    float *htp = hts + p*ST, *htn = hts + (1-p)*ST;
-    dec_l0_kernel<<<256, 256, 0, stream>>>(preZd, dW_ih0, dW_hh0, htp, h0p, c0p, h0t, c0t, t);
-    dec_l1_kernel<<<256, 256, 0, stream>>>(dW_ih1, dW_hh1, db1, h0t, c0t, h1p, c1p,
-                                           h0n, c0n, h1n, c1n, ytb);
-    dec_attn_a<<<768, 256, 0, stream>>>(W_ht2tan, ytb, ench, tanv, scores);
-    dec_attn_b<<<32, 256, 0, stream>>>(tanv, w_tan2pt, scores, encode_len, ench, ctb);
-    dec_attn_c<<<256, 256, 0, stream>>>(W_ct2ht, ctb, ytb, htn, decoutb, t);
-  }
+  megakernel<<<NBLK, TPB, 0, stream>>>(
+      preZe, preZd, eW_hh0, eW_ih1, eW_hh1, eb1,
+      dW_ih0, dW_hh0, dW_ih1, dW_hh1, db1,
+      W_ht2tan, w_tan2pt, W_ct2ht, encode_len,
+      h0, c0, h1, c1, h0t, c0t, ht, ench, tanv, scores, ctb, decoutb,
+      barws + 0, barws + 32);
 
   gemm_mfma<1><<<dim3(16,250), 256, 0, stream>>>(decoutb, HDIM, Wfinb, HDIM, nullptr,
                                                  nullptr, 0, HDIM, rowSum, logitTgt, tokRow);
```

Measured after the change: 27.34 ms. 1.5x slower.
